# Optimization experiments

Hardware: AMD Instinct MI355X
Metric: run time of the kernel (lower is better)

## Reference

```python
import jax, jax.numpy as jnp
import numpy as np

NUM_HEADS = 8
D_HEAD = 64
ATTENTION_WINDOW = 512


def alibi_bias(num_heads, q_len, k_len):
    # ALiBi slopes for power-of-2 number of heads (Press et al. 2021).
    start = 2.0 ** (-(2.0 ** -(np.log2(num_heads) - 3.0)))
    slopes = jnp.asarray([start * (start ** i) for i in range(num_heads)],
                         dtype=jnp.float32)  # [H]
    rel = jnp.arange(q_len)[:, None] - jnp.arange(k_len)[None, :]  # [t, T]
    # Bidirectional ALiBi: bias = -slope * |i - j|
    return -slopes[:, None, None] * jnp.abs(rel).astype(jnp.float32)  # [H, t, T]


def sliding_window_mask(seq_len, window):
    # Attend to tokens within window//2 on each side; even window -> window+1.
    if window % 2 == 0:
        window += 1
    half = window // 2
    idx = jnp.arange(seq_len)
    return jnp.abs(idx[:, None] - idx[None, :]) <= half  # [S, S] bool


def setup_inputs() -> dict:
    key = jax.random.key(0)
    ks = jax.random.split(key, 6)
    B, S, E = 2, 4096, 512
    HD = NUM_HEADS * D_HEAD
    s_in = 1.0 / np.sqrt(E)
    s_out = 1.0 / np.sqrt(HD)
    return {
        'inputs_q': jax.random.normal(ks[0], (B, S, E), jnp.float32),
        'inputs_kv': jax.random.normal(ks[1], (B, S, E), jnp.float32),
        'w_q': jax.random.normal(ks[2], (E, HD), jnp.float32) * s_in,
        'w_k': jax.random.normal(ks[3], (E, HD), jnp.float32) * s_in,
        'w_v': jax.random.normal(ks[4], (E, HD), jnp.float32) * s_in,
        'w_o': jax.random.normal(ks[5], (HD, E), jnp.float32) * s_out,
    }


def reference(inputs_q, inputs_kv, w_q, w_k, w_v, w_o):
    B, S, E = inputs_q.shape
    H, D = NUM_HEADS, D_HEAD
    q = (inputs_q @ w_q).reshape(B, S, H, D)
    k = (inputs_kv @ w_k).reshape(B, S, H, D)
    v = (inputs_kv @ w_v).reshape(B, S, H, D)
    # scores: [B, H, t, T]
    att = jnp.einsum('bthd,bThd->bhtT', q, k) * (1.0 / jnp.sqrt(jnp.float32(D)))
    att = att + alibi_bias(H, S, S)[None]
    mask = sliding_window_mask(S, ATTENTION_WINDOW)
    att = jnp.where(mask[None, None], att, jnp.finfo(jnp.float32).min)
    p = jax.nn.softmax(att, axis=-1)
    out = jnp.einsum('bhtT,bThd->bthd', p, v).reshape(B, S, H * D)
    return out @ w_o
```

## Files before the change

kernel.cpp:

```cpp
#include <hip/hip_runtime.h>

#define S_LEN  4096
#define NH     8
#define DH     64
#define EMB    512
#define HDIM   512
#define HALF_W 256
#define BATCH  2
#define M_ROWS (BATCH * S_LEN)

typedef __attribute__((ext_vector_type(8))) short bf16x8;
typedef __attribute__((ext_vector_type(4))) float f32x4;

__device__ __forceinline__ float b2f(unsigned short u) {
    union { unsigned int i; float f; } v; v.i = ((unsigned int)u) << 16; return v.f;
}
__device__ __forceinline__ unsigned short f2b(float f) {
    unsigned int x = __float_as_uint(f);
    unsigned int r = (x + 0x7fffu + ((x >> 16) & 1u)) >> 16;
    return (unsigned short)r;
}
__device__ __forceinline__ void unpack2(unsigned int u, float* d) {
    d[0] = b2f((unsigned short)(u & 0xffffu));
    d[1] = b2f((unsigned short)(u >> 16));
}
union FragU { uint4 u; bf16x8 f; };
__device__ __forceinline__ bf16x8 ldfrag(const unsigned short* p) {
    FragU x; x.u = *(const uint4*)p; return x.f;
}

__device__ __forceinline__ void async16(const unsigned short* g, unsigned short* l) {
    __builtin_amdgcn_global_load_lds(
        (__attribute__((address_space(1))) void*)const_cast<unsigned short*>(g),
        (__attribute__((address_space(3))) void*)l, 16, 0, 0);
}

__global__ void detect_dtype(const unsigned short* __restrict__ x, int* __restrict__ flag) {
    __shared__ int s;
    if (threadIdx.x == 0) s = 0;
    __syncthreads();
    int bad = 0;
    for (int i = threadIdx.x; i < 2048; i += 256) {
        float v = b2f(x[i]);
        if (!(fabsf(v) < 1.0e6f)) bad = 1;
    }
    if (bad) atomicOr(&s, 1);
    __syncthreads();
    if (threadIdx.x == 0) *flag = s;
}

__global__ __launch_bounds__(256) void transpose_w(
    const void* __restrict__ w0, const void* __restrict__ w1,
    const void* __restrict__ w2, const void* __restrict__ w3,
    unsigned short* __restrict__ out, const int* __restrict__ flag)
{
    __shared__ float t[32][33];
    const int z = blockIdx.z;
    const void* src = (z == 0) ? w0 : (z == 1) ? w1 : (z == 2) ? w2 : w3;
    unsigned short* dst = out + (size_t)z * EMB * EMB;
    const int k0 = blockIdx.y * 32, n0 = blockIdx.x * 32;
    const int kk = threadIdx.x >> 3;
    const int n4 = (threadIdx.x & 7) << 2;
    if (*flag) {
        float4 v = *(const float4*)((const float*)src + (size_t)(k0 + kk) * EMB + n0 + n4);
        t[kk][n4] = v.x; t[kk][n4 + 1] = v.y; t[kk][n4 + 2] = v.z; t[kk][n4 + 3] = v.w;
    } else {
        uint2 u = *(const uint2*)((const unsigned short*)src + (size_t)(k0 + kk) * EMB + n0 + n4);
        unpack2(u.x, &t[kk][n4]); unpack2(u.y, &t[kk][n4 + 2]);
    }
    __syncthreads();
    const int nn = threadIdx.x >> 3;
    const int ks = (threadIdx.x & 7) << 2;
    uint2 pk;
    pk.x = (unsigned int)f2b(t[ks + 0][nn]) | ((unsigned int)f2b(t[ks + 1][nn]) << 16);
    pk.y = (unsigned int)f2b(t[ks + 2][nn]) | ((unsigned int)f2b(t[ks + 3][nn]) << 16);
    *(uint2*)(dst + (size_t)(n0 + nn) * EMB + k0 + ks) = pk;
}

__global__ __launch_bounds__(256) void convert_in(
    const void* __restrict__ xq, const void* __restrict__ xkv,
    unsigned short* __restrict__ Xc, const int* __restrict__ flag)
{
    if (!*flag) return;
    const int z = blockIdx.y;
    const float* src = (const float*)(z ? xkv : xq);
    unsigned short* dst = Xc + (size_t)z * M_ROWS * EMB;
    const size_t base = ((size_t)blockIdx.x * 256 + threadIdx.x) * 8;
    float4 a = *(const float4*)(src + base);
    float4 b = *(const float4*)(src + base + 4);
    uint4 pk;
    pk.x = (unsigned int)f2b(a.x) | ((unsigned int)f2b(a.y) << 16);
    pk.y = (unsigned int)f2b(a.z) | ((unsigned int)f2b(a.w) << 16);
    pk.z = (unsigned int)f2b(b.x) | ((unsigned int)f2b(b.y) << 16);
    pk.w = (unsigned int)f2b(b.z) | ((unsigned int)f2b(b.w) << 16);
    *(uint4*)(dst + base) = pk;
}

__device__ __forceinline__ void mgemm_core4(
    const unsigned short* __restrict__ A, const unsigned short* __restrict__ Bt,
    int m0, f32x4 (*acc)[2],
    unsigned short (*A_lds)[64], unsigned short (*B_lds)[64])
{
    const int tid  = threadIdx.x;
    const int lane = tid & 63;
    const int w    = tid >> 6;
    const int wm   = (w >> 1) << 6;
    const int wn   = (w & 1) << 5;
    const int qcol = lane & 15;
    const int quad = lane >> 4;

    const int srow = tid >> 3;
    const int sp   = tid & 7;

    for (int k0 = 0; k0 < EMB; k0 += 64) {
        __syncthreads();
#pragma unroll
        for (int i = 0; i < 4; ++i) {
            const int row  = (i << 5) + srow;
            const int gcol = ((sp ^ (row & 7)) << 3);
            async16(A + (size_t)(m0 + row) * EMB + k0 + gcol, &A_lds[row][sp << 3]);
        }
#pragma unroll
        for (int i = 0; i < 2; ++i) {
            const int row  = (i << 5) + srow;
            const int gcol = ((sp ^ (row & 7)) << 3);
            async16(Bt + (size_t)row * EMB + k0 + gcol, &B_lds[row][sp << 3]);
        }
        __syncthreads();

#pragma unroll
        for (int kh = 0; kh < 2; ++kh) {
            bf16x8 af[4], bf[2];
#pragma unroll
            for (int i = 0; i < 4; ++i) {
                const int row = wm + (i << 4) + qcol;
                const int p   = ((kh << 2) + quad) ^ (row & 7);
                af[i] = ldfrag(&A_lds[row][p << 3]);
            }
#pragma unroll
            for (int j = 0; j < 2; ++j) {
                const int row = wn + (j << 4) + qcol;
                const int p   = ((kh << 2) + quad) ^ (row & 7);
                bf[j] = ldfrag(&B_lds[row][p << 3]);
            }
#pragma unroll
            for (int i = 0; i < 4; ++i)
#pragma unroll
                for (int j = 0; j < 2; ++j)
                    acc[i][j] = __builtin_amdgcn_mfma_f32_16x16x32_bf16(af[i], bf[j], acc[i][j], 0, 0, 0);
        }
    }
}

__global__ __launch_bounds__(256) void gemm_qkv(
    const void* __restrict__ xq, const void* __restrict__ xkv,
    const unsigned short* __restrict__ Xc, const unsigned short* __restrict__ Wt,
    unsigned short* __restrict__ Qb, unsigned short* __restrict__ Kb,
    unsigned short* __restrict__ Vtb, const int* __restrict__ flag)
{
    __shared__ __align__(16) unsigned short A_lds[128][64];
    __shared__ __align__(16) unsigned short B_lds[64][64];
    const int blk = blockIdx.x;
    const int xcd = blk & 7, idx = blk >> 3;
    const int mi = idx / 24, ni = idx - mi * 24;
    const int m0 = ((xcd << 3) + mi) << 7;
    const int n0 = ni << 6;

    const unsigned short* A;
    if (*flag) A = Xc + (n0 < 512 ? (size_t)0 : (size_t)M_ROWS * EMB);
    else       A = (const unsigned short*)(n0 < 512 ? xq : xkv);
    const unsigned short* Bt = Wt + (size_t)n0 * EMB;

    f32x4 acc[4][2];
#pragma unroll
    for (int i = 0; i < 4; ++i)
#pragma unroll
        for (int j = 0; j < 2; ++j) acc[i][j] = (f32x4){0.f, 0.f, 0.f, 0.f};

    mgemm_core4(A, Bt, m0, acc, A_lds, B_lds);

    const int lane = threadIdx.x & 63, w = threadIdx.x >> 6;
    const int wm = (w >> 1) << 6, wn = (w & 1) << 5;
    const int qcol = lane & 15, quad = lane >> 4;
    const int mode = n0 >> 9;
#pragma unroll
    for (int ms = 0; ms < 4; ++ms)
#pragma unroll
        for (int ns = 0; ns < 2; ++ns)
#pragma unroll
            for (int r = 0; r < 4; ++r) {
                const int m = m0 + wm + (ms << 4) + (quad << 2) + r;
                const int n = n0 + wn + (ns << 4) + qcol;
                const unsigned short us = f2b(acc[ms][ns][r]);
                if (mode == 0) {
                    Qb[(size_t)m * HDIM + n] = us;
                } else if (mode == 1) {
                    Kb[(size_t)m * HDIM + (n - 512)] = us;
                } else {
                    const int hd = n - 1024;
                    const int bb = m >> 12, s = m & (S_LEN - 1);
                    const int hh = hd >> 6, d = hd & 63;
                    Vtb[((size_t)((bb * NH + hh) * DH + d)) * S_LEN + s] = us;
                }
            }
}

__global__ __launch_bounds__(256) void gemm_out(
    const unsigned short* __restrict__ A, const unsigned short* __restrict__ Bt,
    void* __restrict__ C, const int* __restrict__ flag)
{
    __shared__ __align__(16) unsigned short A_lds[128][64];
    __shared__ __align__(16) unsigned short B_lds[64][64];
    const int blk = blockIdx.x;
    const int xcd = blk & 7, idx = blk >> 3;
    const int mi = idx >> 3, ni = idx & 7;
    const int m0 = ((xcd << 3) + mi) << 7;
    const int n0 = ni << 6;

    f32x4 acc[4][2];
#pragma unroll
    for (int i = 0; i < 4; ++i)
#pragma unroll
        for (int j = 0; j < 2; ++j) acc[i][j] = (f32x4){0.f, 0.f, 0.f, 0.f};

    mgemm_core4(A, Bt + (size_t)n0 * EMB, m0, acc, A_lds, B_lds);

    const int lane = threadIdx.x & 63, w = threadIdx.x >> 6;
    const int wm = (w >> 1) << 6, wn = (w & 1) << 5;
    const int qcol = lane & 15, quad = lane >> 4;
    const int fp = *flag;
#pragma unroll
    for (int ms = 0; ms < 4; ++ms)
#pragma unroll
        for (int ns = 0; ns < 2; ++ns)
#pragma unroll
            for (int r = 0; r < 4; ++r) {
                const int m = m0 + wm + (ms << 4) + (quad << 2) + r;
                const int n = n0 + wn + (ns << 4) + qcol;
                const float v = acc[ms][ns][r];
                if (fp) ((float*)C)[(size_t)m * HDIM + n] = v;
                else    ((unsigned short*)C)[(size_t)m * HDIM + n] = f2b(v);
            }
}

__global__ __launch_bounds__(256) void attn_mfma(
    const unsigned short* __restrict__ Q,
    const unsigned short* __restrict__ Kg,
    const unsigned short* __restrict__ Vt,
    unsigned short* __restrict__ O)
{
    __shared__ __align__(16) unsigned short K_lds[64][72];
    __shared__ __align__(16) unsigned short V_lds[64][72];
    __shared__ __align__(16) unsigned short P_lds[4][16][72];

    const int tid  = threadIdx.x;
    const int lane = tid & 63;
    const int w    = tid >> 6;
    const int blk  = blockIdx.x;
    const int bh   = blk >> 6;
    const int r6   = blk & 63;
    const int tile = ((r6 & 7) << 3) | (r6 >> 3);
    const int h    = bh & (NH - 1);
    const int b    = bh >> 3;
    const int t0   = tile << 6;
    const int tq0  = t0 + (w << 4);

    const int qcol = lane & 15;
    const int quad = lane >> 4;
    const float slope = 1.0f / (float)(2 << h);

    const unsigned short* qrow = Q + (size_t)(b * S_LEN + tq0 + qcol) * HDIM + h * DH;
    const bf16x8 qf0 = ldfrag(qrow + quad * 8);
    const bf16x8 qf1 = ldfrag(qrow + 32 + quad * 8);

    f32x4 Oacc[4];
#pragma unroll
    for (int i = 0; i < 4; ++i) Oacc[i] = (f32x4){0.f, 0.f, 0.f, 0.f};
    float lsum = 0.f;

    for (int c = 0; c < 9; ++c) {
        const int j0 = t0 - HALF_W + (c << 6);
        __syncthreads();
#pragma unroll
        for (int p = 0; p < 2; ++p) {
            const int r  = (p << 5) + (tid >> 3);
            const int sg = (tid & 7) << 3;
            const int jc = min(max(j0 + r, 0), S_LEN - 1);
            *(uint4*)&K_lds[r][sg] =
                *(const uint4*)(Kg + (size_t)(b * S_LEN + jc) * HDIM + h * DH + sg);
            const int js = min(max(j0 + sg, 0), S_LEN - 8);
            *(uint4*)&V_lds[r][sg] =
                *(const uint4*)(Vt + ((size_t)((b * NH + h) * DH + r)) * S_LEN + js);
        }
        __syncthreads();

#pragma unroll
        for (int ks = 0; ks < 4; ++ks) {
            const bf16x8 kf0 = ldfrag(&K_lds[(ks << 4) + qcol][quad * 8]);
            const bf16x8 kf1 = ldfrag(&K_lds[(ks << 4) + qcol][32 + quad * 8]);
            f32x4 z = (f32x4){0.f, 0.f, 0.f, 0.f};
            z = __builtin_amdgcn_mfma_f32_16x16x32_bf16(kf0, qf0, z, 0, 0, 0);
            z = __builtin_amdgcn_mfma_f32_16x16x32_bf16(kf1, qf1, z, 0, 0, 0);
            unsigned short pb[4];
#pragma unroll
            for (int r = 0; r < 4; ++r) {
                const int j  = j0 + (ks << 4) + (quad << 2) + r;
                const int dd = (tq0 + qcol) - j;
                const bool ok = (j >= 0) && (j < S_LEN) && (dd <= HALF_W) && (dd >= -HALF_W);
                const float s = z[r] * 0.125f - slope * fabsf((float)dd);
                const float p = ok ? __expf(s - 12.0f) : 0.0f;
                lsum += p;
                pb[r] = f2b(p);
            }
            uint2 pk;
            pk.x = (unsigned int)pb[0] | ((unsigned int)pb[1] << 16);
            pk.y = (unsigned int)pb[2] | ((unsigned int)pb[3] << 16);
            *(uint2*)&P_lds[w][qcol][(ks << 4) + (quad << 2)] = pk;
        }

        const bf16x8 pf0 = ldfrag(&P_lds[w][qcol][quad * 8]);
        const bf16x8 pf1 = ldfrag(&P_lds[w][qcol][32 + quad * 8]);
#pragma unroll
        for (int ds = 0; ds < 4; ++ds) {
            const bf16x8 vf0 = ldfrag(&V_lds[(ds << 4) + qcol][quad * 8]);
            const bf16x8 vf1 = ldfrag(&V_lds[(ds << 4) + qcol][32 + quad * 8]);
            Oacc[ds] = __builtin_amdgcn_mfma_f32_16x16x32_bf16(vf0, pf0, Oacc[ds], 0, 0, 0);
            Oacc[ds] = __builtin_amdgcn_mfma_f32_16x16x32_bf16(vf1, pf1, Oacc[ds], 0, 0, 0);
        }
    }

    lsum += __shfl_xor(lsum, 16, 64);
    lsum += __shfl_xor(lsum, 32, 64);
    const float rz = 1.0f / lsum;

    unsigned short* obase = O + (size_t)(b * S_LEN + tq0 + qcol) * HDIM + h * DH;
#pragma unroll
    for (int ds = 0; ds < 4; ++ds) {
        uint2 pk;
        pk.x = (unsigned int)f2b(Oacc[ds][0] * rz) | ((unsigned int)f2b(Oacc[ds][1] * rz) << 16);
        pk.y = (unsigned int)f2b(Oacc[ds][2] * rz) | ((unsigned int)f2b(Oacc[ds][3] * rz) << 16);
        *(uint2*)(obase + (ds << 4) + (quad << 2)) = pk;
    }
}

extern "C" void kernel_launch(void* const* d_in, const int* in_sizes, int n_in,
                              void* d_out, int out_size, void* d_ws, size_t ws_size,
                              hipStream_t stream) {
    const void* xq  = d_in[0];
    const void* xkv = d_in[1];
    const void* wq  = d_in[2];
    const void* wk  = d_in[3];
    const void* wv  = d_in[4];
    const void* wo  = d_in[5];

    int* flag = (int*)d_ws;
    unsigned short* Qb  = (unsigned short*)((char*)d_ws + 256);
    unsigned short* Kb  = Qb  + (size_t)M_ROWS * HDIM;
    unsigned short* Vtb = Kb  + (size_t)M_ROWS * HDIM;
    unsigned short* Wt  = Vtb + (size_t)M_ROWS * HDIM;
    unsigned short* Wto = Wt + (size_t)3 * EMB * EMB;
    unsigned short* Xc  = (unsigned short*)d_out;

    detect_dtype<<<1, 256, 0, stream>>>((const unsigned short*)xq, flag);
    transpose_w<<<dim3(16, 16, 4), 256, 0, stream>>>(wq, wk, wv, wo, Wt, flag);
    convert_in<<<dim3(2048, 2), 256, 0, stream>>>(xq, xkv, Xc, flag);

    gemm_qkv<<<1536, 256, 0, stream>>>(xq, xkv, Xc, Wt, Qb, Kb, Vtb, flag);
    attn_mfma<<<BATCH * NH * (S_LEN / 64), 256, 0, stream>>>(Qb, Kb, Vtb, Qb);
    gemm_out<<<512, 256, 0, stream>>>(Qb, Wto, d_out, flag);
}
```

Baseline: 170.9 us.

## Widen attention tiles to 128 queries, async swizzled LDS loads, merge prep kernels

The attention kernel now gives each wave 32 query rows instead of 16, so each block covers 128 queries. Every K/V chunk loaded into LDS is reused across twice as many queries, which cuts redundant window loads (10 chunks per 128 queries versus 9 per 64). K/V staging now uses global_load_lds async copies with an XOR swizzle instead of a padded layout. Separately, the dtype detection, weight transpose and input conversion kernels are merged into one prep launch, with each kernel recomputing the flag locally, which trades fewer launches for a small redundant check per block. The attention grid halves to 512 blocks, which may reduce occupancy and latency hiding.

```diff
diff --git a/kernel.cpp b/kernel.cpp
--- a/kernel.cpp
+++ b/kernel.cpp
@@ -35,65 +35,69 @@
         (__attribute__((address_space(3))) void*)l, 16, 0, 0);
 }
 
-__global__ void detect_dtype(const unsigned short* __restrict__ x, int* __restrict__ flag) {
-    __shared__ int s;
-    if (threadIdx.x == 0) s = 0;
+__device__ __forceinline__ int detect_flag(const unsigned short* __restrict__ xq) {
+    __shared__ int s_flag;
+    if (threadIdx.x == 0) s_flag = 0;
     __syncthreads();
+    uint4 u = *(const uint4*)(xq + threadIdx.x * 8);
+    const unsigned short* us = (const unsigned short*)&u;
     int bad = 0;
-    for (int i = threadIdx.x; i < 2048; i += 256) {
-        float v = b2f(x[i]);
+#pragma unroll
+    for (int i = 0; i < 8; ++i) {
+        float v = b2f(us[i]);
         if (!(fabsf(v) < 1.0e6f)) bad = 1;
     }
-    if (bad) atomicOr(&s, 1);
+    if (__any(bad) && (threadIdx.x & 63) == 0) atomicOr(&s_flag, 1);
     __syncthreads();
-    if (threadIdx.x == 0) *flag = s;
-}
-
-__global__ __launch_bounds__(256) void transpose_w(
+    return s_flag;
+}
+
+__global__ __launch_bounds__(256) void prep(
+    const void* __restrict__ xq, const void* __restrict__ xkv,
     const void* __restrict__ w0, const void* __restrict__ w1,
     const void* __restrict__ w2, const void* __restrict__ w3,
-    unsigned short* __restrict__ out, const int* __restrict__ flag)
-{
-    __shared__ float t[32][33];
-    const int z = blockIdx.z;
-    const void* src = (z == 0) ? w0 : (z == 1) ? w1 : (z == 2) ? w2 : w3;
-    unsigned short* dst = out + (size_t)z * EMB * EMB;
-    const int k0 = blockIdx.y * 32, n0 = blockIdx.x * 32;
-    const int kk = threadIdx.x >> 3;
-    const int n4 = (threadIdx.x & 7) << 2;
-    if (*flag) {
-        float4 v = *(const float4*)((const float*)src + (size_t)(k0 + kk) * EMB + n0 + n4);
-        t[kk][n4] = v.x; t[kk][n4 + 1] = v.y; t[kk][n4 + 2] = v.z; t[kk][n4 + 3] = v.w;
+    unsigned short* __restrict__ Wt, unsigned short* __restrict__ Xc)
+{
+    const int flag = detect_flag((const unsigned short*)xq);
+    const int blk = blockIdx.x;
+    if (blk < 1024) {
+        __shared__ float t[32][33];
+        const int z = blk >> 8, idx = blk & 255;
+        const void* src = (z == 0) ? w0 : (z == 1) ? w1 : (z == 2) ? w2 : w3;
+        unsigned short* dst = Wt + (size_t)z * EMB * EMB;
+        const int n0 = (idx & 15) << 5, k0 = (idx >> 4) << 5;
+        const int kk = threadIdx.x >> 3;
+        const int n4 = (threadIdx.x & 7) << 2;
+        if (flag) {
+            float4 v = *(const float4*)((const float*)src + (size_t)(k0 + kk) * EMB + n0 + n4);
+            t[kk][n4] = v.x; t[kk][n4 + 1] = v.y; t[kk][n4 + 2] = v.z; t[kk][n4 + 3] = v.w;
+        } else {
+            uint2 u = *(const uint2*)((const unsigned short*)src + (size_t)(k0 + kk) * EMB + n0 + n4);
+            unpack2(u.x, &t[kk][n4]); unpack2(u.y, &t[kk][n4 + 2]);
+        }
+        __syncthreads();
+        const int nn = threadIdx.x >> 3;
+        const int ks = (threadIdx.x & 7) << 2;
+        uint2 pk;
+        pk.x = (unsigned int)f2b(t[ks + 0][nn]) | ((unsigned int)f2b(t[ks + 1][nn]) << 16);
+        pk.y = (unsigned int)f2b(t[ks + 2][nn]) | ((unsigned int)f2b(t[ks + 3][nn]) << 16);
+        *(uint2*)(dst + (size_t)(n0 + nn) * EMB + k0 + ks) = pk;
     } else {
-        uint2 u = *(const uint2*)((const unsigned short*)src + (size_t)(k0 + kk) * EMB + n0 + n4);
-        unpack2(u.x, &t[kk][n4]); unpack2(u.y, &t[kk][n4 + 2]);
-    }
-    __syncthreads();
-    const int nn = threadIdx.x >> 3;
-    const int ks = (threadIdx.x & 7) << 2;
-    uint2 pk;
-    pk.x = (unsigned int)f2b(t[ks + 0][nn]) | ((unsigned int)f2b(t[ks + 1][nn]) << 16);
-    pk.y = (unsigned int)f2b(t[ks + 2][nn]) | ((unsigned int)f2b(t[ks + 3][nn]) << 16);
-    *(uint2*)(dst + (size_t)(n0 + nn) * EMB + k0 + ks) = pk;
-}
-
-__global__ __launch_bounds__(256) void convert_in(
-    const void* __restrict__ xq, const void* __restrict__ xkv,
-    unsigned short* __restrict__ Xc, const int* __restrict__ flag)
-{
-    if (!*flag) return;
-    const int z = blockIdx.y;
-    const float* src = (const float*)(z ? xkv : xq);
-    unsigned short* dst = Xc + (size_t)z * M_ROWS * EMB;
-    const size_t base = ((size_t)blockIdx.x * 256 + threadIdx.x) * 8;
-    float4 a = *(const float4*)(src + base);
-    float4 b = *(const float4*)(src + base + 4);
-    uint4 pk;
-    pk.x = (unsigned int)f2b(a.x) | ((unsigned int)f2b(a.y) << 16);
-    pk.y = (unsigned int)f2b(a.z) | ((unsigned int)f2b(a.w) << 16);
-    pk.z = (unsigned int)f2b(b.x) | ((unsigned int)f2b(b.y) << 16);
-    pk.w = (unsigned int)f2b(b.z) | ((unsigned int)f2b(b.w) << 16);
-    *(uint4*)(dst + base) = pk;
+        if (!flag) return;
+        const int idx = blk - 1024;
+        const int z = idx >> 11;
+        const float* src = (const float*)(z ? xkv : xq);
+        unsigned short* dst = Xc + (size_t)z * M_ROWS * EMB;
+        const size_t base = ((size_t)(idx & 2047) * 256 + threadIdx.x) * 8;
+        float4 a = *(const float4*)(src + base);
+        float4 b = *(const float4*)(src + base + 4);
+        uint4 pk;
+        pk.x = (unsigned int)f2b(a.x) | ((unsigned int)f2b(a.y) << 16);
+        pk.y = (unsigned int)f2b(a.z) | ((unsigned int)f2b(a.w) << 16);
+        pk.z = (unsigned int)f2b(b.x) | ((unsigned int)f2b(b.y) << 16);
+        pk.w = (unsigned int)f2b(b.z) | ((unsigned int)f2b(b.w) << 16);
+        *(uint4*)(dst + base) = pk;
+    }
 }
 
 __device__ __forceinline__ void mgemm_core4(
@@ -156,8 +160,9 @@
     const void* __restrict__ xq, const void* __restrict__ xkv,
     const unsigned short* __restrict__ Xc, const unsigned short* __restrict__ Wt,
     unsigned short* __restrict__ Qb, unsigned short* __restrict__ Kb,
-    unsigned short* __restrict__ Vtb, const int* __restrict__ flag)
-{
+    unsigned short* __restrict__ Vtb)
+{
+    const int flag = detect_flag((const unsigned short*)xq);
     __shared__ __align__(16) unsigned short A_lds[128][64];
     __shared__ __align__(16) unsigned short B_lds[64][64];
     const int blk = blockIdx.x;
@@ -167,8 +172,8 @@
     const int n0 = ni << 6;
 
     const unsigned short* A;
-    if (*flag) A = Xc + (n0 < 512 ? (size_t)0 : (size_t)M_ROWS * EMB);
-    else       A = (const unsigned short*)(n0 < 512 ? xq : xkv);
+    if (flag) A = Xc + (n0 < 512 ? (size_t)0 : (size_t)M_ROWS * EMB);
+    else      A = (const unsigned short*)(n0 < 512 ? xq : xkv);
     const unsigned short* Bt = Wt + (size_t)n0 * EMB;
 
     f32x4 acc[4][2];
@@ -206,9 +211,11 @@
 }
 
 __global__ __launch_bounds__(256) void gemm_out(
+    const void* __restrict__ xq,
     const unsigned short* __restrict__ A, const unsigned short* __restrict__ Bt,
-    void* __restrict__ C, const int* __restrict__ flag)
-{
+    void* __restrict__ C)
+{
+    const int flag = detect_flag((const unsigned short*)xq);
     __shared__ __align__(16) unsigned short A_lds[128][64];
     __shared__ __align__(16) unsigned short B_lds[64][64];
     const int blk = blockIdx.x;
@@ -228,7 +235,6 @@
     const int lane = threadIdx.x & 63, w = threadIdx.x >> 6;
     const int wm = (w >> 1) << 6, wn = (w & 1) << 5;
     const int qcol = lane & 15, quad = lane >> 4;
-    const int fp = *flag;
 #pragma unroll
     for (int ms = 0; ms < 4; ++ms)
 #pragma unroll
@@ -238,8 +244,8 @@
                 const int m = m0 + wm + (ms << 4) + (quad << 2) + r;
                 const int n = n0 + wn + (ns << 4) + qcol;
                 const float v = acc[ms][ns][r];
-                if (fp) ((float*)C)[(size_t)m * HDIM + n] = v;
-                else    ((unsigned short*)C)[(size_t)m * HDIM + n] = f2b(v);
+                if (flag) ((float*)C)[(size_t)m * HDIM + n] = v;
+                else      ((unsigned short*)C)[(size_t)m * HDIM + n] = f2b(v);
             }
 }
 
@@ -249,97 +255,120 @@
     const unsigned short* __restrict__ Vt,
     unsigned short* __restrict__ O)
 {
-    __shared__ __align__(16) unsigned short K_lds[64][72];
-    __shared__ __align__(16) unsigned short V_lds[64][72];
-    __shared__ __align__(16) unsigned short P_lds[4][16][72];
+    __shared__ __align__(16) unsigned short K_lds[64][64];
+    __shared__ __align__(16) unsigned short V_lds[64][64];
+    __shared__ __align__(16) unsigned short P_lds[4][32][72];
 
     const int tid  = threadIdx.x;
     const int lane = tid & 63;
     const int w    = tid >> 6;
     const int blk  = blockIdx.x;
-    const int bh   = blk >> 6;
-    const int r6   = blk & 63;
-    const int tile = ((r6 & 7) << 3) | (r6 >> 3);
+    const int bh   = blk >> 5;
+    const int r5   = blk & 31;
+    const int tile = ((r5 & 7) << 2) | (r5 >> 3);
     const int h    = bh & (NH - 1);
     const int b    = bh >> 3;
-    const int t0   = tile << 6;
-    const int tq0  = t0 + (w << 4);
+    const int t0   = tile << 7;
+    const int tq0  = t0 + (w << 5);
 
     const int qcol = lane & 15;
     const int quad = lane >> 4;
     const float slope = 1.0f / (float)(2 << h);
 
-    const unsigned short* qrow = Q + (size_t)(b * S_LEN + tq0 + qcol) * HDIM + h * DH;
-    const bf16x8 qf0 = ldfrag(qrow + quad * 8);
-    const bf16x8 qf1 = ldfrag(qrow + 32 + quad * 8);
-
-    f32x4 Oacc[4];
-#pragma unroll
-    for (int i = 0; i < 4; ++i) Oacc[i] = (f32x4){0.f, 0.f, 0.f, 0.f};
-    float lsum = 0.f;
-
-    for (int c = 0; c < 9; ++c) {
+    bf16x8 qf[2][2];
+#pragma unroll
+    for (int qs = 0; qs < 2; ++qs) {
+        const unsigned short* qrow =
+            Q + (size_t)(b * S_LEN + tq0 + (qs << 4) + qcol) * HDIM + h * DH;
+        qf[qs][0] = ldfrag(qrow + quad * 8);
+        qf[qs][1] = ldfrag(qrow + 32 + quad * 8);
+    }
+
+    f32x4 Oacc[2][4];
+#pragma unroll
+    for (int qs = 0; qs < 2; ++qs)
+#pragma unroll
+        for (int i = 0; i < 4; ++i) Oacc[qs][i] = (f32x4){0.f, 0.f, 0.f, 0.f};
+    float lsum[2] = {0.f, 0.f};
+
+    const int srow = tid >> 3;
+    const int sp   = tid & 7;
+
+    for (int c = 0; c < 10; ++c) {
         const int j0 = t0 - HALF_W + (c << 6);
         __syncthreads();
 #pragma unroll
-        for (int p = 0; p < 2; ++p) {
-            const int r  = (p << 5) + (tid >> 3);
-            const int sg = (tid & 7) << 3;
-            const int jc = min(max(j0 + r, 0), S_LEN - 1);
-            *(uint4*)&K_lds[r][sg] =
-                *(const uint4*)(Kg + (size_t)(b * S_LEN + jc) * HDIM + h * DH + sg);
-            const int js = min(max(j0 + sg, 0), S_LEN - 8);
-            *(uint4*)&V_lds[r][sg] =
-                *(const uint4*)(Vt + ((size_t)((b * NH + h) * DH + r)) * S_LEN + js);
-        }
-        __syncthreads();
-
-#pragma unroll
-        for (int ks = 0; ks < 4; ++ks) {
-            const bf16x8 kf0 = ldfrag(&K_lds[(ks << 4) + qcol][quad * 8]);
-            const bf16x8 kf1 = ldfrag(&K_lds[(ks << 4) + qcol][32 + quad * 8]);
-            f32x4 z = (f32x4){0.f, 0.f, 0.f, 0.f};
-            z = __builtin_amdgcn_mfma_f32_16x16x32_bf16(kf0, qf0, z, 0, 0, 0);
-            z = __builtin_amdgcn_mfma_f32_16x16x32_bf16(kf1, qf1, z, 0, 0, 0);
-            unsigned short pb[4];
-#pragma unroll
-            for (int r = 0; r < 4; ++r) {
-                const int j  = j0 + (ks << 4) + (quad << 2) + r;
-                const int dd = (tq0 + qcol) - j;
-                const bool ok = (j >= 0) && (j < S_LEN) && (dd <= HALF_W) && (dd >= -HALF_W);
-                const float s = z[r] * 0.125f - slope * fabsf((float)dd);
-                const float p = ok ? __expf(s - 12.0f) : 0.0f;
-                lsum += p;
-                pb[r] = f2b(p);
-            }
+        for (int i = 0; i < 2; ++i) {
+            const int row  = (i << 5) + srow;
+            const int gseg = (sp ^ (row & 7)) << 3;
+            const int jc = min(max(j0 + row, 0), S_LEN - 1);
+            async16(Kg + (size_t)(b * S_LEN + jc) * HDIM + h * DH + gseg,
+                    &K_lds[row][sp << 3]);
+            const int js = min(max(j0 + gseg, 0), S_LEN - 8);
+            async16(Vt + ((size_t)((b * NH + h) * DH + row)) * S_LEN + js,
+                    &V_lds[row][sp << 3]);
+        }
+        __syncthreads();
+
+#pragma unroll
+        for (int qs = 0; qs < 2; ++qs) {
+#pragma unroll
+            for (int ks = 0; ks < 4; ++ks) {
+                const int krow = (ks << 4) + qcol;
+                const bf16x8 kf0 = ldfrag(&K_lds[krow][(quad ^ (krow & 7)) << 3]);
+                const bf16x8 kf1 = ldfrag(&K_lds[krow][((4 + quad) ^ (krow & 7)) << 3]);
+                f32x4 z = (f32x4){0.f, 0.f, 0.f, 0.f};
+                z = __builtin_amdgcn_mfma_f32_16x16x32_bf16(kf0, qf[qs][0], z, 0, 0, 0);
+                z = __builtin_amdgcn_mfma_f32_16x16x32_bf16(kf1, qf[qs][1], z, 0, 0, 0);
+                unsigned short pb[4];
+#pragma unroll
+                for (int r = 0; r < 4; ++r) {
+                    const int j  = j0 + (ks << 4) + (quad << 2) + r;
+                    const int dd = (tq0 + (qs << 4) + qcol) - j;
+                    const bool ok = (j >= 0) && (j < S_LEN) && (dd <= HALF_W) && (dd >= -HALF_W);
+                    const float s = z[r] * 0.125f - slope * fabsf((float)dd);
+                    const float p = ok ? __expf(s - 12.0f) : 0.0f;
+                    lsum[qs] += p;
+                    pb[r] = f2b(p);
+                }
+                uint2 pk;
+                pk.x = (unsigned int)pb[0] | ((unsigned int)pb[1] << 16);
+                pk.y = (unsigned int)pb[2] | ((unsigned int)pb[3] << 16);
+                *(uint2*)&P_lds[w][(qs << 4) + qcol][(ks << 4) + (quad << 2)] = pk;
+            }
+        }
+#pragma unroll
+        for (int qs = 0; qs < 2; ++qs) {
+            const bf16x8 pf0 = ldfrag(&P_lds[w][(qs << 4) + qcol][quad * 8]);
+            const bf16x8 pf1 = ldfrag(&P_lds[w][(qs << 4) + qcol][32 + quad * 8]);
+#pragma unroll
+            for (int ds = 0; ds < 4; ++ds) {
+                const int vrow = (ds << 4) + qcol;
+                const bf16x8 vf0 = ldfrag(&V_lds[vrow][(quad ^ (vrow & 7)) << 3]);
+                const bf16x8 vf1 = ldfrag(&V_lds[vrow][((4 + quad) ^ (vrow & 7)) << 3]);
+                Oacc[qs][ds] = __builtin_amdgcn_mfma_f32_16x16x32_bf16(vf0, pf0, Oacc[qs][ds], 0, 0, 0);
+                Oacc[qs][ds] = __builtin_amdgcn_mfma_f32_16x16x32_bf16(vf1, pf1, Oacc[qs][ds], 0, 0, 0);
+            }
+        }
+    }
+
+#pragma unroll
+    for (int qs = 0; qs < 2; ++qs) {
+        float l = lsum[qs];
+        l += __shfl_xor(l, 16, 64);
+        l += __shfl_xor(l, 32, 64);
+        const float rz = 1.0f / l;
+        unsigned short* obase =
+            O + (size_t)(b * S_LEN + tq0 + (qs << 4) + qcol) * HDIM + h * DH;
+#pragma unroll
+        for (int ds = 0; ds < 4; ++ds) {
             uint2 pk;
-            pk.x = (unsigned int)pb[0] | ((unsigned int)pb[1] << 16);
-            pk.y = (unsigned int)pb[2] | ((unsigned int)pb[3] << 16);
-            *(uint2*)&P_lds[w][qcol][(ks << 4) + (quad << 2)] = pk;
-        }
-
-        const bf16x8 pf0 = ldfrag(&P_lds[w][qcol][quad * 8]);
-        const bf16x8 pf1 = ldfrag(&P_lds[w][qcol][32 + quad * 8]);
-#pragma unroll
-        for (int ds = 0; ds < 4; ++ds) {
-            const bf16x8 vf0 = ldfrag(&V_lds[(ds << 4) + qcol][quad * 8]);
-            const bf16x8 vf1 = ldfrag(&V_lds[(ds << 4) + qcol][32 + quad * 8]);
-            Oacc[ds] = __builtin_amdgcn_mfma_f32_16x16x32_bf16(vf0, pf0, Oacc[ds], 0, 0, 0);
-            Oacc[ds] = __builtin_amdgcn_mfma_f32_16x16x32_bf16(vf1, pf1, Oacc[ds], 0, 0, 0);
-        }
-    }
-
-    lsum += __shfl_xor(lsum, 16, 64);
-    lsum += __shfl_xor(lsum, 32, 64);
-    const float rz = 1.0f / lsum;
-
-    unsigned short* obase = O + (size_t)(b * S_LEN + tq0 + qcol) * HDIM + h * DH;
-#pragma unroll
-    for (int ds = 0; ds < 4; ++ds) {
-        uint2 pk;
-        pk.x = (unsigned int)f2b(Oacc[ds][0] * rz) | ((unsigned int)f2b(Oacc[ds][1] * rz) << 16);
-        pk.y = (unsigned int)f2b(Oacc[ds][2] * rz) | ((unsigned int)f2b(Oacc[ds][3] * rz) << 16);
-        *(uint2*)(obase + (ds << 4) + (quad << 2)) = pk;
+            pk.x = (unsigned int)f2b(Oacc[qs][ds][0] * rz) |
+                   ((unsigned int)f2b(Oacc[qs][ds][1] * rz) << 16);
+            pk.y = (unsigned int)f2b(Oacc[qs][ds][2] * rz) |
+                   ((unsigned int)f2b(Oacc[qs][ds][3] * rz) << 16);
+            *(uint2*)(obase + (ds << 4) + (quad << 2)) = pk;
+        }
     }
 }
 
@@ -353,7 +382,6 @@
     const void* wv  = d_in[4];
     const void* wo  = d_in[5];
 
-    int* flag = (int*)d_ws;
     unsigned short* Qb  = (unsigned short*)((char*)d_ws + 256);
     unsigned short* Kb  = Qb  + (size_t)M_ROWS * HDIM;
     unsigned short* Vtb = Kb  + (size_t)M_ROWS * HDIM;
@@ -361,11 +389,8 @@
     unsigned short* Wto = Wt + (size_t)3 * EMB * EMB;
     unsigned short* Xc  = (unsigned short*)d_out;
 
-    detect_dtype<<<1, 256, 0, stream>>>((const unsigned short*)xq, flag);
-    transpose_w<<<dim3(16, 16, 4), 256, 0, stream>>>(wq, wk, wv, wo, Wt, flag);
-    convert_in<<<dim3(2048, 2), 256, 0, stream>>>(xq, xkv, Xc, flag);
-
-    gemm_qkv<<<1536, 256, 0, stream>>>(xq, xkv, Xc, Wt, Qb, Kb, Vtb, flag);
-    attn_mfma<<<BATCH * NH * (S_LEN / 64), 256, 0, stream>>>(Qb, Kb, Vtb, Qb);
-    gemm_out<<<512, 256, 0, stream>>>(Qb, Wto, d_out, flag);
-}
+    prep<<<1024 + 4096, 256, 0, stream>>>(xq, xkv, wq, wk, wv, wo, Wt, Xc);
+    gemm_qkv<<<1536, 256, 0, stream>>>(xq, xkv, Xc, Wt, Qb, Kb, Vtb);
+    attn_mfma<<<BATCH * NH * (S_LEN / 128), 256, 0, stream>>>(Qb, Kb, Vtb, Qb);
+    gemm_out<<<512, 256, 0, stream>>>(xq, Qb, Wto, d_out);
+}
```

New measurement: 165.7 us. -3.0%, faster.
